# Optimization experiments

Measured on AMD Instinct MI355X. Metric: run time of the kernel, lower is better.

The kernel has to match this reference:

```python
import jax, jax.numpy as jnp
import numpy as np


def _gcn_norm(edge_index, num_nodes):
    # PyG GCNConv default: add self-loops, symmetric deg^{-1/2} normalization.
    loops = jnp.arange(num_nodes, dtype=edge_index.dtype)
    row = jnp.concatenate([edge_index[0], loops])  # source nodes
    col = jnp.concatenate([edge_index[1], loops])  # target nodes (aggregation)
    deg = jax.ops.segment_sum(jnp.ones_like(col, dtype=jnp.float32), col,
                              num_segments=num_nodes)
    dinv = jnp.where(deg > 0, jax.lax.rsqrt(jnp.maximum(deg, 1.0)), 0.0)
    norm = dinv[row] * dinv[col]  # [E + N]
    return row, col, norm


def _gcn_conv(x, row, col, norm, W, b, num_nodes):
    h = x @ W                                   # [N, F_out] linear first (F_out small)
    msg = norm[:, None] * h[row]                # gather + scale  [E+N, F_out]
    out = jax.ops.segment_sum(msg, col, num_segments=num_nodes)  # scatter-add
    return out + b


def setup_inputs() -> dict:
    key = jax.random.key(0)
    k1, k2, k3, k4, k5, k6, k7 = jax.random.split(key, 7)
    N, E, G = 100000, 3200000, 1024
    in_dim, hidden_dim, out_dim = 2, 32, 32
    x = jax.random.normal(k1, (N, in_dim), dtype=jnp.float32)
    edge_index = jax.random.randint(k2, (2, E), 0, N, dtype=jnp.int64)
    batch = jnp.sort(jax.random.randint(k3, (N,), 0, G, dtype=jnp.int64))
    W1 = jax.random.normal(k4, (in_dim, hidden_dim), dtype=jnp.float32) / np.sqrt(in_dim)
    b1 = jnp.zeros((hidden_dim,), dtype=jnp.float32)
    W2 = jax.random.normal(k5, (hidden_dim, out_dim), dtype=jnp.float32) / np.sqrt(hidden_dim)
    b2 = jnp.zeros((out_dim,), dtype=jnp.float32)
    return {"x": x, "edge_index": edge_index, "batch": batch,
            "num_graphs": G, "W1": W1, "b1": b1, "W2": W2, "b2": b2}


def reference(x, edge_index, batch, num_graphs, W1, b1, W2, b2):
    N = x.shape[0]
    row, col, norm = _gcn_norm(edge_index, N)  # shared across both layers
    h = jax.nn.relu(_gcn_conv(x, row, col, norm, W1, b1, N))
    h = _gcn_conv(h, row, col, norm, W2, b2, N)
    # global_mean_pool over `batch`
    sums = jax.ops.segment_sum(h, batch, num_segments=num_graphs)
    cnts = jax.ops.segment_sum(jnp.ones((N,), dtype=h.dtype), batch,
                               num_segments=num_graphs)
    return sums / jnp.maximum(cnts, 1.0)[:, None]
```

## Files before the change

kernel.cpp:

```cpp
#include <hip/hip_runtime.h>

#define FDIM 32
#define BSHIFT 8
#define CPB (1 << BSHIFT)
#define CMASK (CPB - 1)
#define PAD 16
#define MAXBUK 512
#define BNT 8192
#define BTHREADS 512
#define CTHREADS 512
#define LCAP 13312
#define SENT 0xFFFFFFFFu

__global__ void k_zero(int* __restrict__ bcur, float* __restrict__ pool, int nb, int np) {
    int i = blockIdx.x * blockDim.x + threadIdx.x;
    if (i < nb) bcur[i] = 0;
    if (i < np) pool[i] = 0.0f;
}

__global__ void __launch_bounds__(BTHREADS)
k_binsort(const int* __restrict__ row, const int* __restrict__ col,
          int* bcur, unsigned int* __restrict__ buf, int E, int cap, int NBUK) {
    __shared__ unsigned int lh[MAXBUK];
    __shared__ int lbase[MAXBUK];
    __shared__ int gbase[MAXBUK];
    __shared__ unsigned int swave[4];
    __shared__ unsigned int lpair[BNT];
    int t = threadIdx.x;
    int w = t >> 6, lane = t & 63;
    int base = blockIdx.x * BNT;
    int end = min(base + BNT, E);
    int tilesz = end - base;

    if (t < MAXBUK) lh[t] = 0u;
    __syncthreads();

    int cl[16], rw[16];
    #pragma unroll
    for (int k = 0; k < 4; ++k) {
        int e4 = (base >> 2) + k * BTHREADS + t;
        int eb = 4 * e4;
        if (eb + 3 < end) {
            int4 c4 = *(const int4*)(col + eb);
            int4 r4 = *(const int4*)(row + eb);
            cl[4*k] = c4.x; cl[4*k+1] = c4.y; cl[4*k+2] = c4.z; cl[4*k+3] = c4.w;
            rw[4*k] = r4.x; rw[4*k+1] = r4.y; rw[4*k+2] = r4.z; rw[4*k+3] = r4.w;
            atomicAdd(&lh[c4.x >> BSHIFT], 1u);
            atomicAdd(&lh[c4.y >> BSHIFT], 1u);
            atomicAdd(&lh[c4.z >> BSHIFT], 1u);
            atomicAdd(&lh[c4.w >> BSHIFT], 1u);
        } else {
            #pragma unroll
            for (int q = 0; q < 4; ++q) {
                int e = eb + q;
                if (e < end) {
                    cl[4*k+q] = col[e];
                    rw[4*k+q] = row[e];
                    atomicAdd(&lh[cl[4*k+q] >> BSHIFT], 1u);
                } else cl[4*k+q] = -1;
            }
        }
    }
    __syncthreads();

    if (w < 4) {
        int i0 = w * 128 + lane * 2;
        unsigned int a = lh[i0], b = lh[i0 + 1];
        unsigned int sum = a + b;
        unsigned int sc = sum;
        #pragma unroll
        for (int off = 1; off < 64; off <<= 1) {
            unsigned int u = __shfl_up(sc, off);
            if (lane >= off) sc += u;
        }
        if (lane == 63) swave[w] = sc;
        __syncthreads();
        unsigned int woff = 0;
        for (int k = 0; k < w; ++k) woff += swave[k];
        lbase[i0]     = (int)(woff + sc - sum);
        lbase[i0 + 1] = (int)(woff + sc - sum + a);
    } else {
        __syncthreads();
    }
    __syncthreads();

    for (int bb = t; bb < NBUK; bb += BTHREADS) {
        unsigned int c = lh[bb];
        unsigned int cp = (c + 15u) & ~15u;
        int g = bb * cap + (cp ? atomicAdd(&bcur[bb * PAD], (int)cp) : 0);
        gbase[bb] = g;
        lh[bb] = (unsigned int)g;
    }
    __syncthreads();

    #pragma unroll
    for (int k = 0; k < 16; ++k) {
        if (cl[k] >= 0) {
            int bb = cl[k] >> BSHIFT;
            int gpos = (int)atomicAdd(&lh[bb], 1u);
            int lslot = gpos - gbase[bb] + lbase[bb];
            lpair[lslot] = ((unsigned int)(cl[k] & CMASK) << 24) | (unsigned int)rw[k];
        }
    }
    __syncthreads();

    for (int j = t; j < tilesz; j += BTHREADS) {
        int pos = 0;
        #pragma unroll
        for (int step = 256; step; step >>= 1) {
            int np = pos + step;
            if (np < MAXBUK && lbase[np] <= j) pos = np;
        }
        buf[gbase[pos] + (j - lbase[pos])] = lpair[j];
    }

    for (int bb = t; bb < NBUK; bb += BTHREADS) {
        int lb = lbase[bb];
        int cend = (bb + 1 < NBUK) ? lbase[bb + 1] : tilesz;
        int c = cend - lb;
        int cp = (c + 15) & ~15;
        int g = gbase[bb];
        for (int k = c; k < cp; ++k) buf[g + k] = SENT;
    }
}

__global__ void __launch_bounds__(CTHREADS)
k_csort(unsigned int* __restrict__ buf, const int* __restrict__ bcur,
        int* __restrict__ row_ptr, unsigned int* __restrict__ count,
        const float* __restrict__ x, float* __restrict__ dinv,
        float2* __restrict__ y, float4* __restrict__ triple,
        int cap, int N) {
    __shared__ unsigned int lp[LCAP];
    __shared__ unsigned int lh[CPB];
    __shared__ int lofs[CPB];
    __shared__ unsigned int swave[4];
    int b = blockIdx.x;
    int t = threadIdx.x;
    int w = t >> 6, lane = t & 63;
    int c0 = b << BSHIFT;
    int s = b * cap;
    int cntb = bcur[b * PAD];
    if (t < CPB) lh[t] = 0u;
    if (b == 0 && t == 0) {
        y[N] = make_float2(0.0f, 0.0f);
        triple[N] = make_float4(0.0f, 0.0f, 0.0f, 0.0f);
    }
    __syncthreads();
    for (int j = t; j < cntb; j += CTHREADS) {
        unsigned int u = buf[s + j];
        lp[j] = u;
        if (u != SENT) atomicAdd(&lh[u >> 24], 1u);
    }
    __syncthreads();
    unsigned int v = 0, pv = 0, sc = 0;
    int i0 = (w << 6) | lane;
    if (w < 4) {
        v = lh[i0];
        pv = (v + 7u) & ~7u;
        sc = pv;
        #pragma unroll
        for (int off = 1; off < 64; off <<= 1) {
            unsigned int u = __shfl_up(sc, off);
            if (lane >= off) sc += u;
        }
        if (lane == 63) swave[w] = sc;
    }
    __syncthreads();
    int myexcl = 0;
    if (w < 4) {
        unsigned int woff = 0;
        for (int k = 0; k < w; ++k) woff += swave[k];
        myexcl = s + (int)(woff + sc - pv);
        int c = c0 + i0;
        if (c < N) {
            row_ptr[c] = myexcl;
            count[c] = v;
            float dv = rsqrtf((float)v + 1.0f);
            dinv[c] = dv;
            float2 xv = ((const float2*)x)[c];
            y[c] = make_float2(dv * xv.x, dv * xv.y);
        }
        lofs[i0] = myexcl;
    }
    __syncthreads();
    for (int j = t; j < cntb; j += CTHREADS) {
        unsigned int u = lp[j];
        if (u != SENT) {
            int pos = atomicAdd(&lofs[u >> 24], 1);
            buf[pos] = u & 0x00FFFFFFu;
        }
    }
    __syncthreads();
    if (w < 4) {
        for (unsigned int k = v; k < pv; ++k) buf[myexcl + k] = (unsigned int)N;
    }
}


__global__ void k_prep(const float* __restrict__ x, const unsigned int* __restrict__ count,
                       float* __restrict__ dinv, float2* __restrict__ y,
                       float4* __restrict__ triple, int N) {
    int i = blockIdx.x * blockDim.x + threadIdx.x;
    if (i == 0) {
        y[N] = make_float2(0.0f, 0.0f);
        triple[N] = make_float4(0.0f, 0.0f, 0.0f, 0.0f);
    }
    if (i >= N) return;
    float dv = rsqrtf((float)count[i] + 1.0f);
    dinv[i] = dv;
    float2 xv = ((const float2*)x)[i];
    y[i] = make_float2(dv * xv.x, dv * xv.y);
}

__global__ void k_agg1(const int* __restrict__ row_ptr, const unsigned int* __restrict__ count,
                       const int* __restrict__ sorted_row, const float2* __restrict__ y,
                       const float* __restrict__ dinv, float4* __restrict__ triple, int N) {
    int t = threadIdx.x;
    int i = blockIdx.x * 32 + (t >> 3), l = t & 7;
    if (i >= N) return;
    int s = row_ptr[i];
    int e = s + (int)count[i];
    float zx = 0.0f, zy = 0.0f;
    for (int j = s + l; j < e; j += 8) {
        float2 yv = y[sorted_row[j]];
        zx += yv.x; zy += yv.y;
    }
    #pragma unroll
    for (int m = 4; m >= 1; m >>= 1) {
        zx += __shfl_xor(zx, m);
        zy += __shfl_xor(zy, m);
    }
    if (l == 0) {
        float2 yi = y[i];
        zx += yi.x; zy += yi.y;
        float dv = dinv[i];
        triple[i] = make_float4(dv * zx, dv * zy, dv, 0.0f);
    }
}

__device__ __forceinline__ float4 f4fma(float s, float4 m, float4 a) {
    return make_float4(fmaf(s, m.x, a.x), fmaf(s, m.y, a.y),
                       fmaf(s, m.z, a.z), fmaf(s, m.w, a.w));
}
__device__ __forceinline__ float4 f4relu(float4 q) {
    return make_float4(fmaxf(q.x, 0.f), fmaxf(q.y, 0.f), fmaxf(q.z, 0.f), fmaxf(q.w, 0.f));
}
#define EDGE_TERM(tt) acc = f4fma((tt).z, f4relu(f4fma((tt).x, w0, f4fma((tt).y, w1, bb))), acc)

__global__ void __launch_bounds__(256)
k_agg_pool(const int* __restrict__ row_ptr, const unsigned int* __restrict__ count,
           const int* __restrict__ sorted_row, const float4* __restrict__ triple,
           const float* __restrict__ W1, const float* __restrict__ b1,
           const int* __restrict__ batch, float* __restrict__ pool,
           float* __restrict__ cnt, int N) {
    __shared__ float sh[32][FDIM];
    __shared__ int sb[32];
    int t = threadIdx.x;
    int n = t >> 3, l = t & 7;
    int i = blockIdx.x * 32 + n;
    int fa = 4 * l;
    float4 w0 = *(const float4*)(W1 + fa);
    float4 w1 = *(const float4*)(W1 + FDIM + fa);
    float4 bb = *(const float4*)(b1 + fa);
    float4 acc = make_float4(0.f, 0.f, 0.f, 0.f);
    int bt = -1;
    if (i < N) {
        float4 ts = triple[i];
        float dv = ts.z;
        EDGE_TERM(ts);
        int s = row_ptr[i];
        int pv = ((int)count[i] + 7) & ~7;
        int end16 = s + (pv & ~15);
        int j = s;
        for (; j < end16; j += 16) {
            int4 ra = *(const int4*)(sorted_row + j);
            int4 rb = *(const int4*)(sorted_row + j + 4);
            int4 rc = *(const int4*)(sorted_row + j + 8);
            int4 rd = *(const int4*)(sorted_row + j + 12);
            float4 t0 = triple[ra.x], t1 = triple[ra.y], t2 = triple[ra.z], t3 = triple[ra.w];
            float4 t4 = triple[rb.x], t5 = triple[rb.y], t6 = triple[rb.z], t7 = triple[rb.w];
            float4 t8 = triple[rc.x], t9 = triple[rc.y], ta = triple[rc.z], tb = triple[rc.w];
            float4 tc = triple[rd.x], td = triple[rd.y], te = triple[rd.z], tf = triple[rd.w];
            EDGE_TERM(t0); EDGE_TERM(t1); EDGE_TERM(t2); EDGE_TERM(t3);
            EDGE_TERM(t4); EDGE_TERM(t5); EDGE_TERM(t6); EDGE_TERM(t7);
            EDGE_TERM(t8); EDGE_TERM(t9); EDGE_TERM(ta); EDGE_TERM(tb);
            EDGE_TERM(tc); EDGE_TERM(td); EDGE_TERM(te); EDGE_TERM(tf);
        }
        if (pv & 8) {
            int4 ra = *(const int4*)(sorted_row + j);
            int4 rb = *(const int4*)(sorted_row + j + 4);
            float4 t0 = triple[ra.x], t1 = triple[ra.y], t2 = triple[ra.z], t3 = triple[ra.w];
            float4 t4 = triple[rb.x], t5 = triple[rb.y], t6 = triple[rb.z], t7 = triple[rb.w];
            EDGE_TERM(t0); EDGE_TERM(t1); EDGE_TERM(t2); EDGE_TERM(t3);
            EDGE_TERM(t4); EDGE_TERM(t5); EDGE_TERM(t6); EDGE_TERM(t7);
        }
        acc.x *= dv; acc.y *= dv; acc.z *= dv; acc.w *= dv;
        bt = batch[i];
    }
    *(float4*)&sh[n][fa] = acc;
    if (l == 0) sb[n] = bt;
    __syncthreads();
    if (bt >= 0 && (n == 0 || sb[n - 1] != bt)) {
        float4 ssum = acc;
        int m = n + 1;
        for (; m < 32 && sb[m] == bt; ++m) {
            float4 o = *(const float4*)&sh[m][fa];
            ssum.x += o.x; ssum.y += o.y; ssum.z += o.z; ssum.w += o.w;
        }
        atomicAdd(&pool[bt * FDIM + fa],     ssum.x);
        atomicAdd(&pool[bt * FDIM + fa + 1], ssum.y);
        atomicAdd(&pool[bt * FDIM + fa + 2], ssum.z);
        atomicAdd(&pool[bt * FDIM + fa + 3], ssum.w);
        if (l == 0) atomicAdd(&cnt[bt], (float)(m - n));
    }
}

__global__ void k_out(const float* __restrict__ pool, const float* __restrict__ cnt,
                      const float* __restrict__ W2, const float* __restrict__ b2,
                      float* __restrict__ out, int G) {
    __shared__ float sW[FDIM * FDIM];
    int t = threadIdx.x;
    for (int k = t; k < FDIM * FDIM; k += 256) sW[k] = W2[k];
    __syncthreads();
    int g = blockIdx.x * 8 + (t >> 5), f = t & 31;
    if (g >= G) return;
    float c = cnt[g];
    float o = 0.0f;
    if (c > 0.0f) {
        float s = 0.0f;
        #pragma unroll
        for (int k = 0; k < FDIM; ++k) s = fmaf(pool[g * FDIM + k], sW[k * FDIM + f], s);
        o = fmaf(s, 1.0f / c, b2[f]);
    }
    out[g * FDIM + f] = o;
}


__global__ void k_fhist(const int* __restrict__ col, unsigned int* __restrict__ count, int E) {
    int i = blockIdx.x * blockDim.x + threadIdx.x;
    if (i < E) atomicAdd(&count[col[i]], 1u);
}
__global__ void k_fsc2(const int* __restrict__ row, const int* __restrict__ col,
                       const float2* __restrict__ y, float* __restrict__ z, int E) {
    int e = blockIdx.x * blockDim.x + threadIdx.x;
    if (e >= E) return;
    float2 yv = y[row[e]];
    int c = col[e];
    atomicAdd(&z[2 * c],     yv.x);
    atomicAdd(&z[2 * c + 1], yv.y);
}
__global__ void k_fmkt(const float* __restrict__ z, const float2* __restrict__ y,
                       const float* __restrict__ dinv, float4* __restrict__ triple, int N) {
    int i = blockIdx.x * blockDim.x + threadIdx.x;
    if (i >= N) return;
    float dv = dinv[i];
    float2 yi = y[i];
    triple[i] = make_float4(dv * (z[2 * i] + yi.x), dv * (z[2 * i + 1] + yi.y), dv, 0.0f);
}
__global__ void k_fsc32(const int* __restrict__ row, const int* __restrict__ col,
                        const float4* __restrict__ triple, const float* __restrict__ W1,
                        const float* __restrict__ b1, float* __restrict__ v, int total) {
    int idx = blockIdx.x * blockDim.x + threadIdx.x;
    if (idx >= total) return;
    int e = idx >> 5, f = idx & 31;
    float4 tr = triple[row[e]];
    float u = tr.z * fmaxf(fmaf(tr.x, W1[f], fmaf(tr.y, W1[FDIM + f], b1[f])), 0.0f);
    atomicAdd(&v[col[e] * FDIM + f], u);
}
__global__ void k_ffin(const float4* __restrict__ triple, const float* __restrict__ v,
                       const float* __restrict__ W1, const float* __restrict__ b1,
                       const int* __restrict__ batch, float* __restrict__ pool,
                       float* __restrict__ cnt, int N) {
    int idx = blockIdx.x * blockDim.x + threadIdx.x;
    int i = idx >> 5, f = idx & 31;
    if (i >= N) return;
    float4 tr = triple[i];
    float u = tr.z * fmaxf(fmaf(tr.x, W1[f], fmaf(tr.y, W1[FDIM + f], b1[f])), 0.0f);
    float w = tr.z * (u + v[i * FDIM + f]);
    int b = batch[i];
    atomicAdd(&pool[b * FDIM + f], w);
    if (f == 0) atomicAdd(&cnt[b], 1.0f);
}

extern "C" void kernel_launch(void* const* d_in, const int* in_sizes, int n_in,
                              void* d_out, int out_size, void* d_ws, size_t ws_size,
                              hipStream_t stream) {
    const float* x   = (const float*)d_in[0];
    const int*   ei  = (const int*)d_in[1];
    const int* batch = (const int*)d_in[2];
    const float* W1  = (const float*)d_in[4];
    const float* b1  = (const float*)d_in[5];
    const float* W2  = (const float*)d_in[6];
    const float* b2  = (const float*)d_in[7];
    float* out = (float*)d_out;

    int N = in_sizes[0] / 2;
    int E = in_sizes[1] / 2;
    int G = out_size / FDIM;

    const int* row = ei;
    const int* col = ei + E;

    int NB = (N + 255) / 256;
    int NBUK = (N + CMASK) >> BSHIFT;
    int ntiles = (E + BNT - 1) / BNT;

    int capBase = (E + NBUK - 1) / NBUK;
    int cap = capBase + ntiles * 8 + 1536;
    cap = (cap + 15) & ~15;

    size_t off = 0;
    size_t o_bcur = off;  off += (size_t)NBUK * PAD;
    size_t o_cnt  = off;  off += N;
    size_t o_rp   = off;  off += N;
    size_t o_dv   = off;  off += N;
    size_t o_y    = off;  off += 2ull * (N + 1);
    off = (off + 3) & ~(size_t)3;
    size_t o_tr   = off;  off += 4ull * (N + 1);
    size_t o_buf  = off;  off += (size_t)NBUK * cap;
    size_t o_pool = off;  off += 32ull * G;
    size_t o_cg   = off;  off += G;
    size_t elemsNew = off;

    unsigned int* W = (unsigned int*)d_ws;

    if (ws_size >= elemsNew * 4 && N < (1 << 24) && NBUK <= MAXBUK && cap <= LCAP) {
        int* bcur           = (int*)(W + o_bcur);
        unsigned int* count = (unsigned int*)(W + o_cnt);
        int* row_ptr        = (int*)(W + o_rp);
        float* dinv         = (float*)(W + o_dv);
        float2* y           = (float2*)(W + o_y);
        float4* triple      = (float4*)(W + o_tr);
        unsigned int* buf   = W + o_buf;
        float* pool         = (float*)(W + o_pool);
        float* cntg         = (float*)(W + o_cg);

        int nb = NBUK * PAD;
        int np = G * FDIM + G;
        int zgrid = (max(nb, np) + 255) / 256;
        k_zero<<<zgrid, 256, 0, stream>>>(bcur, pool, nb, np);

        k_binsort<<<ntiles, BTHREADS, 0, stream>>>(row, col, bcur, buf, E, cap, NBUK);
        k_csort<<<NBUK, CTHREADS, 0, stream>>>(buf, bcur, row_ptr, count, x, dinv, y, triple, cap, N);

        k_agg1<<<(N + 31) / 32, 256, 0, stream>>>(row_ptr, count, (const int*)buf, y, dinv,
                                                  triple, N);
        k_agg_pool<<<(N + 31) / 32, 256, 0, stream>>>(row_ptr, count, (const int*)buf, triple,
                                                      W1, b1, batch, pool, cntg, N);
        k_out<<<(G + 7) / 8, 256, 0, stream>>>(pool, cntg, W2, b2, out, G);
    } else {
        unsigned int* count = (unsigned int*)d_ws;
        float* dinv         = (float*)(count + N);
        float2* y           = (float2*)(dinv + N);
        float* z            = (float*)(y + N + 1);
        size_t toff = ((size_t)(z + 2 * N - (float*)d_ws) + 3) & ~(size_t)3;
        float4* triple      = (float4*)((float*)d_ws + toff);
        float* v            = (float*)(triple + N + 1);
        float* pool         = v + 32ull * N;
        float* cntg         = pool + 32ull * G;

        hipMemsetAsync(count, 0, (size_t)N * 4, stream);
        hipMemsetAsync(z, 0, (size_t)N * 8, stream);
        hipMemsetAsync(v, 0, (size_t)N * FDIM * 4, stream);
        hipMemsetAsync(pool, 0, (size_t)(G * FDIM + G) * 4, stream);

        k_fhist<<<(E + 255) / 256, 256, 0, stream>>>(col, count, E);
        k_prep<<<NB, 256, 0, stream>>>(x, count, dinv, y, triple, N);
        k_fsc2<<<(E + 255) / 256, 256, 0, stream>>>(row, col, y, z, E);
        k_fmkt<<<NB, 256, 0, stream>>>(z, y, dinv, triple, N);
        int ts = E * FDIM;
        k_fsc32<<<(ts + 255) / 256, 256, 0, stream>>>(row, col, triple, W1, b1, v, ts);
        k_ffin<<<(N * FDIM + 255) / 256, 256, 0, stream>>>(triple, v, W1, b1, batch, pool, cntg, N);
        k_out<<<(G + 7) / 8, 256, 0, stream>>>(pool, cntg, W2, b2, out, G);
    }
}
```

Measured before the change: 120.0 us.

## Size binsort tiles to one tile per CU and unroll agg1 gather loop

The binsort kernel now takes a runtime tile size of about E/256 edges, giving roughly 256 blocks, where before it used fixed 8192-edge tiles (about 390 blocks for this input). Edges are streamed twice from global memory, once to build the histogram and once to scatter, instead of being held in registers. Larger tiles mean fewer global bucket atomics and less per-block padding, at the cost of reading the edge list twice and using more shared memory. Separately, the agg1 gather loop is unrolled by two and relies on padded bucket slots with sentinel entries so it needs no per-element bounds checks.

```diff
diff --git a/kernel.cpp b/kernel.cpp
--- a/kernel.cpp
+++ b/kernel.cpp
@@ -6,9 +6,9 @@
 #define CMASK (CPB - 1)
 #define PAD 16
 #define MAXBUK 512
-#define BNT 8192
 #define BTHREADS 512
 #define CTHREADS 512
+#define LPMAX 12544
 #define LCAP 13312
 #define SENT 0xFFFFFFFFu
 
@@ -20,47 +20,31 @@
 
 __global__ void __launch_bounds__(BTHREADS)
 k_binsort(const int* __restrict__ row, const int* __restrict__ col,
-          int* bcur, unsigned int* __restrict__ buf, int E, int cap, int NBUK) {
+          int* bcur, unsigned int* __restrict__ buf, int E, int bnt, int cap, int NBUK) {
     __shared__ unsigned int lh[MAXBUK];
     __shared__ int lbase[MAXBUK];
     __shared__ int gbase[MAXBUK];
     __shared__ unsigned int swave[4];
-    __shared__ unsigned int lpair[BNT];
+    __shared__ unsigned int lpair[LPMAX];
     int t = threadIdx.x;
     int w = t >> 6, lane = t & 63;
-    int base = blockIdx.x * BNT;
-    int end = min(base + BNT, E);
+    int base = blockIdx.x * bnt;
+    int end = min(base + bnt, E);
     int tilesz = end - base;
-
-    if (t < MAXBUK) lh[t] = 0u;
-    __syncthreads();
-
-    int cl[16], rw[16];
-    #pragma unroll
-    for (int k = 0; k < 4; ++k) {
-        int e4 = (base >> 2) + k * BTHREADS + t;
-        int eb = 4 * e4;
-        if (eb + 3 < end) {
-            int4 c4 = *(const int4*)(col + eb);
-            int4 r4 = *(const int4*)(row + eb);
-            cl[4*k] = c4.x; cl[4*k+1] = c4.y; cl[4*k+2] = c4.z; cl[4*k+3] = c4.w;
-            rw[4*k] = r4.x; rw[4*k+1] = r4.y; rw[4*k+2] = r4.z; rw[4*k+3] = r4.w;
-            atomicAdd(&lh[c4.x >> BSHIFT], 1u);
-            atomicAdd(&lh[c4.y >> BSHIFT], 1u);
-            atomicAdd(&lh[c4.z >> BSHIFT], 1u);
-            atomicAdd(&lh[c4.w >> BSHIFT], 1u);
-        } else {
-            #pragma unroll
-            for (int q = 0; q < 4; ++q) {
-                int e = eb + q;
-                if (e < end) {
-                    cl[4*k+q] = col[e];
-                    rw[4*k+q] = row[e];
-                    atomicAdd(&lh[cl[4*k+q] >> BSHIFT], 1u);
-                } else cl[4*k+q] = -1;
-            }
-        }
-    }
+    int nq = tilesz >> 2;
+    int rem = tilesz & 3;
+
+    lh[t] = 0u;
+    __syncthreads();
+
+    for (int q = t; q < nq; q += BTHREADS) {
+        int4 c4 = *(const int4*)(col + base + 4 * q);
+        atomicAdd(&lh[c4.x >> BSHIFT], 1u);
+        atomicAdd(&lh[c4.y >> BSHIFT], 1u);
+        atomicAdd(&lh[c4.z >> BSHIFT], 1u);
+        atomicAdd(&lh[c4.w >> BSHIFT], 1u);
+    }
+    if (t < rem) atomicAdd(&lh[col[base + (nq << 2) + t] >> BSHIFT], 1u);
     __syncthreads();
 
     if (w < 4) {
@@ -93,14 +77,27 @@
     }
     __syncthreads();
 
-    #pragma unroll
-    for (int k = 0; k < 16; ++k) {
-        if (cl[k] >= 0) {
-            int bb = cl[k] >> BSHIFT;
+    for (int q = t; q < nq; q += BTHREADS) {
+        int eb = base + 4 * q;
+        int4 c4 = *(const int4*)(col + eb);
+        int4 r4 = *(const int4*)(row + eb);
+        int cc[4] = {c4.x, c4.y, c4.z, c4.w};
+        int rr[4] = {r4.x, r4.y, r4.z, r4.w};
+        #pragma unroll
+        for (int k = 0; k < 4; ++k) {
+            int bb = cc[k] >> BSHIFT;
             int gpos = (int)atomicAdd(&lh[bb], 1u);
             int lslot = gpos - gbase[bb] + lbase[bb];
-            lpair[lslot] = ((unsigned int)(cl[k] & CMASK) << 24) | (unsigned int)rw[k];
-        }
+            lpair[lslot] = ((unsigned int)(cc[k] & CMASK) << 24) | (unsigned int)rr[k];
+        }
+    }
+    if (t < rem) {
+        int e = base + (nq << 2) + t;
+        int c = col[e];
+        int bb = c >> BSHIFT;
+        int gpos = (int)atomicAdd(&lh[bb], 1u);
+        int lslot = gpos - gbase[bb] + lbase[bb];
+        lpair[lslot] = ((unsigned int)(c & CMASK) << 24) | (unsigned int)row[e];
     }
     __syncthreads();
 
@@ -219,11 +216,22 @@
     int i = blockIdx.x * 32 + (t >> 3), l = t & 7;
     if (i >= N) return;
     int s = row_ptr[i];
-    int e = s + (int)count[i];
+    int pv = ((int)count[i] + 7) & ~7;
     float zx = 0.0f, zy = 0.0f;
-    for (int j = s + l; j < e; j += 8) {
-        float2 yv = y[sorted_row[j]];
-        zx += yv.x; zy += yv.y;
+    int end16 = s + (pv & ~15);
+    int j = s;
+    for (; j < end16; j += 16) {
+        int i0 = sorted_row[j + l];
+        int i1 = sorted_row[j + 8 + l];
+        float2 a = y[i0];
+        float2 b = y[i1];
+        zx += a.x; zy += a.y;
+        zx += b.x; zy += b.y;
+    }
+    if (pv & 8) {
+        int i0 = sorted_row[j + l];
+        float2 a = y[i0];
+        zx += a.x; zy += a.y;
     }
     #pragma unroll
     for (int m = 4; m >= 1; m >>= 1) {
@@ -403,7 +411,10 @@
 
     int NB = (N + 255) / 256;
     int NBUK = (N + CMASK) >> BSHIFT;
-    int ntiles = (E + BNT - 1) / BNT;
+
+    int bnt = (E + 255) / 256;
+    bnt = (bnt + 15) & ~15;
+    int ntiles = (E + bnt - 1) / bnt;
 
     int capBase = (E + NBUK - 1) / NBUK;
     int cap = capBase + ntiles * 8 + 1536;
@@ -424,7 +435,8 @@
 
     unsigned int* W = (unsigned int*)d_ws;
 
-    if (ws_size >= elemsNew * 4 && N < (1 << 24) && NBUK <= MAXBUK && cap <= LCAP) {
+    if (ws_size >= elemsNew * 4 && N < (1 << 24) && NBUK <= MAXBUK &&
+        cap <= LCAP && bnt <= LPMAX && (E & 3) == 0) {
         int* bcur           = (int*)(W + o_bcur);
         unsigned int* count = (unsigned int*)(W + o_cnt);
         int* row_ptr        = (int*)(W + o_rp);
@@ -440,7 +452,7 @@
         int zgrid = (max(nb, np) + 255) / 256;
         k_zero<<<zgrid, 256, 0, stream>>>(bcur, pool, nb, np);
 
-        k_binsort<<<ntiles, BTHREADS, 0, stream>>>(row, col, bcur, buf, E, cap, NBUK);
+        k_binsort<<<ntiles, BTHREADS, 0, stream>>>(row, col, bcur, buf, E, bnt, cap, NBUK);
         k_csort<<<NBUK, CTHREADS, 0, stream>>>(buf, bcur, row_ptr, count, x, dinv, y, triple, cap, N);
 
         k_agg1<<<(N + 31) / 32, 256, 0, stream>>>(row_ptr, count, (const int*)buf, y, dinv,
```

Result: faster. 115.8 us (-3.5%).
